# Optimization experiments

Measured on AMD Instinct MI355X. Metric: run time of the kernel, lower is better.

The kernel has to match this reference:

```python
import jax, jax.numpy as jnp
import numpy as np

E = 200_000       # num edges
A = 1_000_000     # num angle triplets
H = 128           # hidden_dim
BD = 8            # bilinear_dim
NR = 6            # num_radial_basis
NS = 7            # num_spherical_basis
MIN = 128         # message_in_dim
N_BEFORE = 1
N_AFTER = 2


def setup_inputs() -> dict:
    key = jax.random.key(0)
    ks = jax.random.split(key, 24)
    s = 0.05
    inp = {
        "distance_representation": jax.random.normal(ks[0], (E, NR), jnp.float32),
        "angle_representation": jax.random.normal(ks[1], (A, NS, NR), jnp.float32),
        "message": jax.random.normal(ks[2], (E, MIN), jnp.float32),
        "angle_index": jax.random.randint(ks[3], (2, A), 0, E),
        # parameters (stored as [in, out]; torch Linear applies x @ W.T)
        "W_dist": jax.random.normal(ks[4], (NR, H), jnp.float32) * s,
        "W_angle": jax.random.normal(ks[5], (NS * NR, BD), jnp.float32) * s,
        "W_src": jax.random.normal(ks[6], (MIN, H), jnp.float32) * s,
        "b_src": jnp.zeros((H,), jnp.float32),
        "W_tgt": jax.random.normal(ks[7], (MIN, H), jnp.float32) * s,
        "b_tgt": jnp.zeros((H,), jnp.float32),
        "W_bil": jax.random.normal(ks[8], (H, BD, H), jnp.float32) * (2.0 / H),
        "res_before_W": jax.random.normal(ks[9], (N_BEFORE, 2, H, H), jnp.float32) * s,
        "res_before_b": jnp.zeros((N_BEFORE, 2, H), jnp.float32),
        "W_skip": jax.random.normal(ks[10], (H, MIN), jnp.float32) * s,
        "b_skip": jnp.zeros((MIN,), jnp.float32),
        "res_after_W": jax.random.normal(ks[11], (N_AFTER, 2, MIN, MIN), jnp.float32) * s,
        "res_after_b": jnp.zeros((N_AFTER, 2, MIN), jnp.float32),
    }
    return inp


def _residual(x, Ws, bs, act):
    # x + act(L2(act(L1(x))))
    h = act(x @ Ws[0] + bs[0])
    h = act(h @ Ws[1] + bs[1])
    return x + h


def reference(distance_representation, angle_representation, message, angle_index,
              W_dist, W_angle, W_src, b_src, W_tgt, b_tgt, W_bil,
              res_before_W, res_before_b, W_skip, b_skip,
              res_after_W, res_after_b):
    act = jax.nn.silu
    num_edges = message.shape[0]
    num_angles = angle_index.shape[-1]

    d = distance_representation @ W_dist                       # [E, H]
    a = angle_representation.reshape(num_angles, -1) @ W_angle  # [A, BD]

    src_e, tgt_e = angle_index[0], angle_index[1]
    sm = message[src_e] @ W_src + b_src                        # [A, H] gather + linear
    sm = sm * d[tgt_e]                                         # [A, H]
    sm = jnp.einsum('ab,ah,ibh->ai', a, sm, W_bil)             # [A, H] bilinear

    agg = jax.ops.segment_sum(sm, tgt_e, num_segments=num_edges)  # [E, H] scatter-add

    x0 = message
    x = agg + (message @ W_tgt + b_tgt)
    for i in range(res_before_W.shape[0]):
        x = _residual(x, res_before_W[i], res_before_b[i], act)
    x = act(x @ W_skip + b_skip) + x0
    for i in range(res_after_W.shape[0]):
        x = _residual(x, res_after_W[i], res_after_b[i], act)
    return x
```

## Files before the change

### kernel.cpp

```cpp
#include <hip/hip_runtime.h>
#include <stdint.h>

#define E_N 200000
#define A_N 1000000

typedef short s16x8 __attribute__((ext_vector_type(8)));
typedef short s16x4 __attribute__((ext_vector_type(4)));
typedef float f32x4 __attribute__((ext_vector_type(4)));
typedef uint32_t u32x4 __attribute__((ext_vector_type(4)));
typedef uint32_t u32x2 __attribute__((ext_vector_type(2)));

__device__ __forceinline__ ushort f2bf(float f) {
  uint32_t x = __float_as_uint(f);
  uint32_t r = x + 0x7FFFu + ((x >> 16) & 1u);
  return (ushort)(r >> 16);
}

__device__ __forceinline__ float bf2f(ushort u) {
  return __uint_as_float(((uint32_t)u) << 16);
}

__device__ __forceinline__ uint32_t cvtpk(float lo, float hi) {
  uint32_t r;
  asm("v_cvt_pk_bf16_f32 %0, %1, %2" : "=v"(r) : "v"(lo), "v"(hi));
  return r;
}

__device__ __forceinline__ float silu_f(float v) {
  return v * (1.0f / (1.0f + __expf(-v)));
}

__device__ __forceinline__ int swz(int row, int h) {
  return row * 128 + (h ^ ((row & 7) << 3));
}

__device__ __forceinline__ int sws(int r, int c) {
  return r * 64 + ((c & 63) ^ ((r & 7) << 3));
}

__device__ __forceinline__ void exchCtoB(ushort* scw, int r15, int hi,
                                         const f32x4* xv, s16x8* st) {
  u32x2 pk[8];
#pragma unroll
  for (int nt = 0; nt < 8; nt++) {
    pk[nt][0] = cvtpk(xv[nt][0], xv[nt][1]);
    pk[nt][1] = cvtpk(xv[nt][2], xv[nt][3]);
  }
#pragma unroll
  for (int nt = 0; nt < 4; nt++)
    *(u32x2*)&scw[sws(r15, nt * 16 + hi * 4)] = pk[nt];
#pragma unroll
  for (int k = 0; k < 2; k++)
    st[k] = *(const s16x8*)&scw[sws(r15, k * 32 + hi * 8)];
#pragma unroll
  for (int nt = 4; nt < 8; nt++)
    *(u32x2*)&scw[sws(r15, nt * 16 + hi * 4)] = pk[nt];
#pragma unroll
  for (int k = 2; k < 4; k++)
    st[k] = *(const s16x8*)&scw[sws(r15, k * 32 + hi * 8)];
}

__device__ __forceinline__ void exchBtoC(ushort* scw, int r15, int hi,
                                         const s16x8* stv, u32x2* mc) {
#pragma unroll
  for (int k = 0; k < 2; k++)
    *(s16x8*)&scw[sws(r15, k * 32 + hi * 8)] = stv[k];
#pragma unroll
  for (int nt = 0; nt < 4; nt++)
    mc[nt] = *(const u32x2*)&scw[sws(r15, nt * 16 + hi * 4)];
#pragma unroll
  for (int k = 2; k < 4; k++)
    *(s16x8*)&scw[sws(r15, k * 32 + hi * 8)] = stv[k];
#pragma unroll
  for (int nt = 4; nt < 8; nt++)
    mc[nt] = *(const u32x2*)&scw[sws(r15, nt * 16 + hi * 4)];
}

__global__ __launch_bounds__(256) void k_prep(
    const float* __restrict__ Wbil, const float* __restrict__ Wsrc,
    const float* __restrict__ Wtgt, const float* __restrict__ WresB,
    const float* __restrict__ Wskip, const float* __restrict__ WresA,
    const float* __restrict__ bsrc, const float* __restrict__ btgt,
    const float* __restrict__ bresB, const float* __restrict__ bskip,
    const float* __restrict__ bresA,
    ushort* __restrict__ wg_bil, ushort* __restrict__ wg_lin,
    float* __restrict__ bias_tab) {
  int tid = blockIdx.x * 256 + threadIdx.x;
  if (tid < 8 * 16384) {
    int b = tid >> 14, r = tid & 16383;
    int i = r >> 7, h = r & 127;
    wg_bil[b * 16384 + swz(i, h)] = f2bf(Wbil[(i * 8 + b) * 128 + h]);
    return;
  }
  tid -= 8 * 16384;
  if (tid < 9 * 16384) {
    int s = tid >> 14, r = tid & 16383;
    int c = r >> 7, h = r & 127;
    const float* src;
    switch (s) {
      case 0: src = Wsrc; break;
      case 1: src = Wtgt; break;
      case 2: src = WresB; break;
      case 3: src = WresB + 16384; break;
      case 4: src = Wskip; break;
      case 5: src = WresA; break;
      case 6: src = WresA + 16384; break;
      case 7: src = WresA + 32768; break;
      default: src = WresA + 49152; break;
    }
    wg_lin[s * 16384 + swz(c, h)] = f2bf(src[h * 128 + c]);
    return;
  }
  tid -= 9 * 16384;
  if (tid < 9 * 128) {
    int s = tid >> 7, c = tid & 127;
    const float* src;
    switch (s) {
      case 0: src = bsrc; break;
      case 1: src = btgt; break;
      case 2: src = bresB; break;
      case 3: src = bresB + 128; break;
      case 4: src = bskip; break;
      case 5: src = bresA; break;
      case 6: src = bresA + 128; break;
      case 7: src = bresA + 256; break;
      default: src = bresA + 384; break;
    }
    bias_tab[s * 128 + c] = src[c];
  }
}

__global__ __launch_bounds__(256) void k_hist(const int* __restrict__ aidx,
                                              int* __restrict__ cnt) {
  int i = blockIdx.x * 256 + threadIdx.x;
  if (i < A_N) atomicAdd(&cnt[aidx[A_N + i]], 1);
}

__global__ __launch_bounds__(256) void k_scan1(const int* __restrict__ cnt,
                                               int* __restrict__ excl,
                                               int* __restrict__ bsum) {
  __shared__ int s[256];
  int t = threadIdx.x;
  int base = blockIdx.x * 1024 + t * 4;
  int v[4];
#pragma unroll
  for (int j = 0; j < 4; j++) v[j] = (base + j < E_N) ? cnt[base + j] : 0;
  int sum = v[0] + v[1] + v[2] + v[3];
  s[t] = sum;
  __syncthreads();
#pragma unroll
  for (int d = 1; d < 256; d <<= 1) {
    int x = (t >= d) ? s[t - d] : 0;
    __syncthreads();
    s[t] += x;
    __syncthreads();
  }
  int run = s[t] - sum;
#pragma unroll
  for (int j = 0; j < 4; j++) {
    if (base + j < E_N) excl[base + j] = run;
    run += v[j];
  }
  if (t == 255) bsum[blockIdx.x] = s[255];
}

__global__ __launch_bounds__(256) void k_scan2(int* __restrict__ bsum, int nb) {
  __shared__ int s[256];
  int t = threadIdx.x;
  int orig = (t < nb) ? bsum[t] : 0;
  s[t] = orig;
  __syncthreads();
#pragma unroll
  for (int d = 1; d < 256; d <<= 1) {
    int x = (t >= d) ? s[t - d] : 0;
    __syncthreads();
    s[t] += x;
    __syncthreads();
  }
  if (t < nb) bsum[t] = s[t] - orig;
}

__global__ __launch_bounds__(256) void k_scan3(const int* __restrict__ excl,
                                               const int* __restrict__ bsum,
                                               int* __restrict__ cursor) {
  int t = threadIdx.x;
  int base = blockIdx.x * 1024 + t * 4;
  int add = bsum[blockIdx.x];
#pragma unroll
  for (int j = 0; j < 4; j++)
    if (base + j < E_N) cursor[base + j] = excl[base + j] + add;
}

__global__ __launch_bounds__(256) void k_scatter(const int* __restrict__ aidx,
                                                 int* __restrict__ cursor,
                                                 int* __restrict__ perm,
                                                 int* __restrict__ ste) {
  int i = blockIdx.x * 256 + threadIdx.x;
  if (i < A_N) {
    int te = aidx[A_N + i];
    int pos = atomicAdd(&cursor[te], 1);
    perm[pos] = i;
    ste[pos] = te;
  }
}

__global__ __launch_bounds__(256) void k_angle(const float* __restrict__ ang,
                                               const float* __restrict__ Wang,
                                               float* __restrict__ a_ws) {
  __shared__ float rows[128 * 42];
  __shared__ float wbuf[42 * 8];
  int t = threadIdx.x;
  int tile0 = blockIdx.x * 128;
  int nrows = A_N - tile0; if (nrows > 128) nrows = 128;
  if (nrows == 128) {
    const f32x4* src = (const f32x4*)(ang + (size_t)tile0 * 42);
    f32x4* dst = (f32x4*)rows;
    for (int k = t; k < 1344; k += 256) dst[k] = src[k];
  } else {
    int cnt = nrows * 42;
    for (int k = t; k < cnt; k += 256) rows[k] = ang[(size_t)tile0 * 42 + k];
  }
  for (int k = t; k < 336; k += 256) wbuf[k] = Wang[k];
  __syncthreads();
  int row = t >> 1, half = t & 1;
  if (row < nrows) {
    float a0 = 0.f, a1 = 0.f, a2 = 0.f, a3 = 0.f;
    const float* rp = &rows[row * 42];
    const float* wp = &wbuf[half * 4];
#pragma unroll
    for (int k = 0; k < 42; k++) {
      float v = rp[k];
      a0 += v * wp[k * 8 + 0]; a1 += v * wp[k * 8 + 1];
      a2 += v * wp[k * 8 + 2]; a3 += v * wp[k * 8 + 3];
    }
    f32x4 o; o.x = a0; o.y = a1; o.z = a2; o.w = a3;
    *(f32x4*)&a_ws[(tile0 + row) * 8 + half * 4] = o;
  }
}

__global__ __launch_bounds__(256) void k_dist(const float* __restrict__ dist,
                                              const float* __restrict__ Wd,
                                              ushort* __restrict__ dtab) {
  __shared__ float w[6 * 128];
  int t = threadIdx.x;
  for (int k = t; k < 768; k += 256) w[k] = Wd[k];
  __syncthreads();
  int gid = blockIdx.x * 256 + t;
  int e = gid >> 2, q = gid & 3;
  if (e >= E_N) return;
  float dv[6];
#pragma unroll
  for (int r = 0; r < 6; r++) dv[r] = dist[e * 6 + r];
#pragma unroll
  for (int j = 0; j < 32; j += 4) {
    int c = q * 32 + j;
    s16x4 o;
#pragma unroll
    for (int jj = 0; jj < 4; jj++) {
      float s = 0.f;
#pragma unroll
      for (int r = 0; r < 6; r++) s += dv[r] * w[r * 128 + c + jj];
      o[jj] = (short)f2bf(s);
    }
    *(s16x4*)&dtab[e * 128 + c] = o;
  }
}

__global__ __launch_bounds__(512) void k_srcm(const float* __restrict__ msg,
                                              const ushort* __restrict__ wg_lin,
                                              const float* __restrict__ bias_tab,
                                              ushort* __restrict__ srcm) {
  __shared__ ushort xb[128 * 128];
  __shared__ ushort wb[16384];
  __shared__ float bias[128];
  int t = threadIdx.x;
  int tile0 = blockIdx.x * 128;
  const f32x4 Z4 = {0.f, 0.f, 0.f, 0.f};
  for (int off = t * 8; off < 16384; off += 4096)
    *(s16x8*)&wb[off] = *(const s16x8*)&wg_lin[off];
  if (t < 128) bias[t] = bias_tab[t];
  {
    int row = t >> 2, l = t & 3;
    int grow = tile0 + row;
#pragma unroll
    for (int j = 0; j < 8; j++) {
      int h = l * 32 + j * 4;
      s16x4 o; o[0] = 0; o[1] = 0; o[2] = 0; o[3] = 0;
      if (grow < E_N) {
        f32x4 v = *(const f32x4*)&msg[(size_t)grow * 128 + h];
        o[0] = (short)f2bf(v.x); o[1] = (short)f2bf(v.y);
        o[2] = (short)f2bf(v.z); o[3] = (short)f2bf(v.w);
      }
      *(s16x4*)&xb[swz(row, h)] = o;
    }
  }
  __syncthreads();
  int w = t >> 6, lane = t & 63;
  int rbase = w * 16;
  int arow = rbase + (lane & 15);
  int k0 = (lane >> 4) * 8;
  int r0 = (lane >> 4) * 4;
  f32x4 acc[8];
#pragma unroll
  for (int k = 0; k < 4; k++) {
    s16x8 af = *(const s16x8*)&xb[swz(arow, k * 32 + k0)];
#pragma unroll
    for (int nt = 0; nt < 8; nt++) {
      s16x8 bf = *(const s16x8*)&wb[swz(nt * 16 + (lane & 15), k * 32 + k0)];
      acc[nt] = __builtin_amdgcn_mfma_f32_16x16x32_bf16(af, bf, k == 0 ? Z4 : acc[nt], 0, 0, 0);
    }
  }
#pragma unroll
  for (int nt = 0; nt < 8; nt++) {
    int col = nt * 16 + (lane & 15);
    float bv = bias[col];
#pragma unroll
    for (int r = 0; r < 4; r++) {
      int grow = tile0 + rbase + r0 + r;
      if (grow < E_N) srcm[(size_t)grow * 128 + col] = f2bf(acc[nt][r] + bv);
    }
  }
}

__global__ __launch_bounds__(256) void k_bil(const int* __restrict__ aidx,
                                             const ushort* __restrict__ srcm,
                                             const ushort* __restrict__ dtab,
                                             const float* __restrict__ a_ws,
                                             const ushort* __restrict__ wg_bil,
                                             const int* __restrict__ perm,
                                             const int* __restrict__ ste,
                                             float* __restrict__ agg) {
  __shared__ ushort wb[2][16384];
  int t = threadIdx.x;
  int lane = t & 63, w = t >> 6;
  int tile0 = blockIdx.x * 128;
  int mb = w * 32;
  int r15 = lane & 15, hi = lane >> 4;
  int k0 = hi * 8;
  int r0 = hi * 4;
  const f32x4 Z4 = {0.f, 0.f, 0.f, 0.f};

  {
    const ushort* gs = wg_bil + w * 4096 + lane * 8;
    ushort* ls = &wb[0][w * 4096];
#pragma unroll
    for (int i = 0; i < 8; i++)
      __builtin_amdgcn_global_load_lds(
          (const __attribute__((address_space(1))) void*)(gs + i * 512),
          (__attribute__((address_space(3))) void*)(ls + i * 512), 16, 0, 0);
  }

  float smv[2][4][8];
  float av[2][8];
  int teo[2][4];
#pragma unroll
  for (int mt = 0; mt < 2; mt++) {
    int grow = tile0 + mb + mt * 16 + r15;
    int ok = (grow < A_N);
    int ga = ok ? perm[grow] : 0;
    int se = ok ? aidx[ga] : 0;
    int te = ok ? ste[grow] : 0;
    if (ok) {
      f32x4 a0 = *(const f32x4*)&a_ws[(size_t)ga * 8];
      f32x4 a1 = *(const f32x4*)&a_ws[(size_t)ga * 8 + 4];
#pragma unroll
      for (int j = 0; j < 4; j++) { av[mt][j] = a0[j]; av[mt][4 + j] = a1[j]; }
    } else {
#pragma unroll
      for (int j = 0; j < 8; j++) av[mt][j] = 0.f;
    }
#pragma unroll
    for (int k = 0; k < 4; k++) {
      s16x8 sv = *(const s16x8*)&srcm[(size_t)se * 128 + k * 32 + k0];
      s16x8 dv = *(const s16x8*)&dtab[(size_t)te * 128 + k * 32 + k0];
#pragma unroll
      for (int j = 0; j < 8; j++)
        smv[mt][k][j] = bf2f((ushort)sv[j]) * bf2f((ushort)dv[j]);
    }
#pragma unroll
    for (int r = 0; r < 4; r++) {
      int orow = tile0 + mb + mt * 16 + r0 + r;
      teo[mt][r] = (orow < A_N) ? ste[orow] : 0;
    }
  }

  f32x4 OUT[2][8];
#pragma unroll
  for (int mt = 0; mt < 2; mt++)
#pragma unroll
    for (int nt = 0; nt < 8; nt++) OUT[mt][nt] = Z4;

  __syncthreads();

#pragma unroll
  for (int b = 0; b < 8; b++) {
    int buf = b & 1;
    if (b < 7) {
      const ushort* gs = wg_bil + (b + 1) * 16384 + w * 4096 + lane * 8;
      ushort* ls = &wb[buf ^ 1][w * 4096];
#pragma unroll
      for (int i = 0; i < 8; i++)
        __builtin_amdgcn_global_load_lds(
            (const __attribute__((address_space(1))) void*)(gs + i * 512),
            (__attribute__((address_space(3))) void*)(ls + i * 512), 16, 0, 0);
    }
    float a0b = av[0][b], a1b = av[1][b];
#pragma unroll
    for (int k = 0; k < 4; k++) {
      u32x4 w0, w1;
#pragma unroll
      for (int jj = 0; jj < 4; jj++) {
        w0[jj] = cvtpk(a0b * smv[0][k][2 * jj], a0b * smv[0][k][2 * jj + 1]);
        w1[jj] = cvtpk(a1b * smv[1][k][2 * jj], a1b * smv[1][k][2 * jj + 1]);
      }
      s16x8 af0 = __builtin_bit_cast(s16x8, w0);
      s16x8 af1 = __builtin_bit_cast(s16x8, w1);
#pragma unroll
      for (int nt = 0; nt < 8; nt++) {
        s16x8 bf = *(const s16x8*)&wb[buf][swz(nt * 16 + r15, k * 32 + k0)];
        OUT[0][nt] = __builtin_amdgcn_mfma_f32_16x16x32_bf16(af0, bf, OUT[0][nt], 0, 0, 0);
        OUT[1][nt] = __builtin_amdgcn_mfma_f32_16x16x32_bf16(af1, bf, OUT[1][nt], 0, 0, 0);
      }
    }
    __syncthreads();
  }

#pragma unroll
  for (int mt = 0; mt < 2; mt++) {
    float acc[8];
    int cte = teo[mt][0];
#pragma unroll
    for (int nt = 0; nt < 8; nt++) acc[nt] = OUT[mt][nt][0];
#pragma unroll
    for (int r = 1; r < 4; r++) {
      int nte = teo[mt][r];
      if (nte == cte) {
#pragma unroll
        for (int nt = 0; nt < 8; nt++) acc[nt] += OUT[mt][nt][r];
      } else {
        float* base = &agg[(size_t)cte * 128];
#pragma unroll
        for (int nt = 0; nt < 8; nt++)
          unsafeAtomicAdd(base + nt * 16 + r15, acc[nt]);
        cte = nte;
#pragma unroll
        for (int nt = 0; nt < 8; nt++) acc[nt] = OUT[mt][nt][r];
      }
    }
    float* base = &agg[(size_t)cte * 128];
#pragma unroll
    for (int nt = 0; nt < 8; nt++)
      unsafeAtomicAdd(base + nt * 16 + r15, acc[nt]);
  }
}

__global__ __launch_bounds__(512) void k_postA(const float* __restrict__ msg,
                                               const float* __restrict__ agg,
                                               const ushort* __restrict__ wg_lin,
                                               const float* __restrict__ bias_tab,
                                               ushort* __restrict__ xmid) {
  __shared__ ushort wb[4][16384];
  __shared__ ushort sc[8][1024];
  __shared__ float bias[4][128];
  int t = threadIdx.x;
  int lane = t & 63, w = t >> 6;
  int r15 = lane & 15, hi = lane >> 4;
  ushort* scw = &sc[w][0];
  const f32x4 Z4 = {0.f, 0.f, 0.f, 0.f};

#pragma unroll
  for (int s = 0; s < 4; s++) {
    const ushort* gs = wg_lin + (s + 1) * 16384 + t * 8;
    ushort* ls = &wb[s][t * 8];
#pragma unroll
    for (int i = 0; i < 4; i++)
      __builtin_amdgcn_global_load_lds(
          (const __attribute__((address_space(1))) void*)(gs + i * 4096),
          (__attribute__((address_space(3))) void*)(ls + i * 4096), 16, 0, 0);
  }
  if (t < 128) {
#pragma unroll
    for (int s = 0; s < 4; s++) bias[s][t] = bias_tab[(s + 1) * 128 + t];
  }
  __syncthreads();

#pragma unroll 1
  for (int tb = blockIdx.x; tb < 1563; tb += 521) {
    int r = tb * 128 + w * 16 + r15;
    bool ok = r < E_N;
    size_t gb = (size_t)r * 128;

    s16x8 st[4], mg[4];
#pragma unroll
    for (int k = 0; k < 4; k++) {
      f32x4 v0 = Z4, v1 = Z4;
      if (ok) {
        v0 = *(const f32x4*)&msg[gb + k * 32 + hi * 8];
        v1 = *(const f32x4*)&msg[gb + k * 32 + hi * 8 + 4];
      }
      u32x4 p;
      p[0] = cvtpk(v0.x, v0.y); p[1] = cvtpk(v0.z, v0.w);
      p[2] = cvtpk(v1.x, v1.y); p[3] = cvtpk(v1.z, v1.w);
      st[k] = __builtin_bit_cast(s16x8, p);
      mg[k] = st[k];
    }
    f32x4 ag[8];
#pragma unroll
    for (int nt = 0; nt < 8; nt++)
      ag[nt] = ok ? *(const f32x4*)&agg[gb + nt * 16 + hi * 4] : Z4;

    f32x4 xr[8], xv[8], C[8];

#pragma unroll
    for (int k = 0; k < 4; k++)
#pragma unroll
      for (int nt = 0; nt < 8; nt++) {
        s16x8 af = *(const s16x8*)&wb[0][swz(nt * 16 + r15, k * 32 + hi * 8)];
        C[nt] = __builtin_amdgcn_mfma_f32_16x16x32_bf16(af, st[k], k == 0 ? ag[nt] : C[nt], 0, 0, 0);
      }
#pragma unroll
    for (int nt = 0; nt < 8; nt++) {
      f32x4 bv = *(const f32x4*)&bias[0][nt * 16 + hi * 4];
#pragma unroll
      for (int q = 0; q < 4; q++) xv[nt][q] = C[nt][q] + bv[q];
      xr[nt] = xv[nt];
    }
    exchCtoB(scw, r15, hi, xv, st);

#pragma unroll
    for (int k = 0; k < 4; k++)
#pragma unroll
      for (int nt = 0; nt < 8; nt++) {
        s16x8 af = *(const s16x8*)&wb[1][swz(nt * 16 + r15, k * 32 + hi * 8)];
        C[nt] = __builtin_amdgcn_mfma_f32_16x16x32_bf16(af, st[k], k == 0 ? Z4 : C[nt], 0, 0, 0);
      }
#pragma unroll
    for (int nt = 0; nt < 8; nt++) {
      f32x4 bv = *(const f32x4*)&bias[1][nt * 16 + hi * 4];
#pragma unroll
      for (int q = 0; q < 4; q++) xv[nt][q] = silu_f(C[nt][q] + bv[q]);
    }
    exchCtoB(scw, r15, hi, xv, st);

#pragma unroll
    for (int k = 0; k < 4; k++)
#pragma unroll
      for (int nt = 0; nt < 8; nt++) {
        s16x8 af = *(const s16x8*)&wb[2][swz(nt * 16 + r15, k * 32 + hi * 8)];
        C[nt] = __builtin_amdgcn_mfma_f32_16x16x32_bf16(af, st[k], k == 0 ? Z4 : C[nt], 0, 0, 0);
      }
#pragma unroll
    for (int nt = 0; nt < 8; nt++) {
      f32x4 bv = *(const f32x4*)&bias[2][nt * 16 + hi * 4];
#pragma unroll
      for (int q = 0; q < 4; q++) xv[nt][q] = xr[nt][q] + silu_f(C[nt][q] + bv[q]);
    }
    exchCtoB(scw, r15, hi, xv, st);

#pragma unroll
    for (int k = 0; k < 4; k++)
#pragma unroll
      for (int nt = 0; nt < 8; nt++) {
        s16x8 af = *(const s16x8*)&wb[3][swz(nt * 16 + r15, k * 32 + hi * 8)];
        C[nt] = __builtin_amdgcn_mfma_f32_16x16x32_bf16(af, st[k], k == 0 ? Z4 : C[nt], 0, 0, 0);
      }
    u32x2 mc[8];
    exchBtoC(scw, r15, hi, mg, mc);
#pragma unroll
    for (int nt = 0; nt < 8; nt++) {
      f32x4 bv = *(const f32x4*)&bias[3][nt * 16 + hi * 4];
      f32x4 m0;
      m0[0] = __uint_as_float(mc[nt][0] << 16);
      m0[1] = __uint_as_float(mc[nt][0] & 0xffff0000u);
      m0[2] = __uint_as_float(mc[nt][1] << 16);
      m0[3] = __uint_as_float(mc[nt][1] & 0xffff0000u);
      u32x2 pk;
      float o0 = silu_f(C[nt][0] + bv[0]) + m0[0];
      float o1 = silu_f(C[nt][1] + bv[1]) + m0[1];
      float o2 = silu_f(C[nt][2] + bv[2]) + m0[2];
      float o3 = silu_f(C[nt][3] + bv[3]) + m0[3];
      pk[0] = cvtpk(o0, o1);
      pk[1] = cvtpk(o2, o3);
      if (ok) *(u32x2*)&xmid[gb + nt * 16 + hi * 4] = pk;
    }
  }
}

__global__ __launch_bounds__(512) void k_postB(const ushort* __restrict__ xmid,
                                               const ushort* __restrict__ wg_lin,
                                               const float* __restrict__ bias_tab,
                                               float* __restrict__ xout) {
  __shared__ ushort wb[4][16384];
  __shared__ ushort sc[8][1024];
  __shared__ float bias[4][128];
  int t = threadIdx.x;
  int lane = t & 63, w = t >> 6;
  int r15 = lane & 15, hi = lane >> 4;
  ushort* scw = &sc[w][0];
  const f32x4 Z4 = {0.f, 0.f, 0.f, 0.f};

#pragma unroll
  for (int s = 0; s < 4; s++) {
    const ushort* gs = wg_lin + (s + 5) * 16384 + t * 8;
    ushort* ls = &wb[s][t * 8];
#pragma unroll
    for (int i = 0; i < 4; i++)
      __builtin_amdgcn_global_load_lds(
          (const __attribute__((address_space(1))) void*)(gs + i * 4096),
          (__attribute__((address_space(3))) void*)(ls + i * 4096), 16, 0, 0);
  }
  if (t < 128) {
#pragma unroll
    for (int s = 0; s < 4; s++) bias[s][t] = bias_tab[(s + 5) * 128 + t];
  }
  __syncthreads();

#pragma unroll 1
  for (int tb = blockIdx.x; tb < 1563; tb += 521) {
    int r = tb * 128 + w * 16 + r15;
    bool ok = r < E_N;
    size_t gb = (size_t)r * 128;

    s16x8 st[4];
#pragma unroll
    for (int k = 0; k < 4; k++) {
      s16x8 z; u32x4 zz; zz[0] = 0; zz[1] = 0; zz[2] = 0; zz[3] = 0;
      z = __builtin_bit_cast(s16x8, zz);
      st[k] = ok ? *(const s16x8*)&xmid[gb + k * 32 + hi * 8] : z;
    }
    u32x2 mc[8];
    exchBtoC(scw, r15, hi, st, mc);
    f32x4 xr[8], xv[8], C[8];
#pragma unroll
    for (int nt = 0; nt < 8; nt++) {
      xr[nt][0] = __uint_as_float(mc[nt][0] << 16);
      xr[nt][1] = __uint_as_float(mc[nt][0] & 0xffff0000u);
      xr[nt][2] = __uint_as_float(mc[nt][1] << 16);
      xr[nt][3] = __uint_as_float(mc[nt][1] & 0xffff0000u);
    }

#pragma unroll
    for (int k = 0; k < 4; k++)
#pragma unroll
      for (int nt = 0; nt < 8; nt++) {
        s16x8 af = *(const s16x8*)&wb[0][swz(nt * 16 + r15, k * 32 + hi * 8)];
        C[nt] = __builtin_amdgcn_mfma_f32_16x16x32_bf16(af, st[k], k == 0 ? Z4 : C[nt], 0, 0, 0);
      }
#pragma unroll
    for (int nt = 0; nt < 8; nt++) {
      f32x4 bv = *(const f32x4*)&bias[0][nt * 16 + hi * 4];
#pragma unroll
      for (int q = 0; q < 4; q++) xv[nt][q] = silu_f(C[nt][q] + bv[q]);
    }
    exchCtoB(scw, r15, hi, xv, st);

#pragma unroll
    for (int k = 0; k < 4; k++)
#pragma unroll
      for (int nt = 0; nt < 8; nt++) {
        s16x8 af = *(const s16x8*)&wb[1][swz(nt * 16 + r15, k * 32 + hi * 8)];
        C[nt] = __builtin_amdgcn_mfma_f32_16x16x32_bf16(af, st[k], k == 0 ? Z4 : C[nt], 0, 0, 0);
      }
#pragma unroll
    for (int nt = 0; nt < 8; nt++) {
      f32x4 bv = *(const f32x4*)&bias[1][nt * 16 + hi * 4];
#pragma unroll
      for (int q = 0; q < 4; q++) xv[nt][q] = xr[nt][q] + silu_f(C[nt][q] + bv[q]);
      xr[nt] = xv[nt];
    }
    exchCtoB(scw, r15, hi, xv, st);

#pragma unroll
    for (int k = 0; k < 4; k++)
#pragma unroll
      for (int nt = 0; nt < 8; nt++) {
        s16x8 af = *(const s16x8*)&wb[2][swz(nt * 16 + r15, k * 32 + hi * 8)];
        C[nt] = __builtin_amdgcn_mfma_f32_16x16x32_bf16(af, st[k], k == 0 ? Z4 : C[nt], 0, 0, 0);
      }
#pragma unroll
    for (int nt = 0; nt < 8; nt++) {
      f32x4 bv = *(const f32x4*)&bias[2][nt * 16 + hi * 4];
#pragma unroll
      for (int q = 0; q < 4; q++) xv[nt][q] = silu_f(C[nt][q] + bv[q]);
    }
    exchCtoB(scw, r15, hi, xv, st);

#pragma unroll
    for (int k = 0; k < 4; k++)
#pragma unroll
      for (int nt = 0; nt < 8; nt++) {
        s16x8 af = *(const s16x8*)&wb[3][swz(nt * 16 + r15, k * 32 + hi * 8)];
        C[nt] = __builtin_amdgcn_mfma_f32_16x16x32_bf16(af, st[k], k == 0 ? Z4 : C[nt], 0, 0, 0);
      }
#pragma unroll
    for (int nt = 0; nt < 8; nt++) {
      f32x4 bv = *(const f32x4*)&bias[3][nt * 16 + hi * 4];
      f32x4 o;
#pragma unroll
      for (int q = 0; q < 4; q++) o[q] = xr[nt][q] + silu_f(C[nt][q] + bv[q]);
      if (ok) *(f32x4*)&xout[gb + nt * 16 + hi * 4] = o;
    }
  }
}

extern "C" void kernel_launch(void* const* d_in, const int* in_sizes, int n_in,
                              void* d_out, int out_size, void* d_ws, size_t ws_size,
                              hipStream_t stream) {
  const float* dist  = (const float*)d_in[0];
  const float* ang   = (const float*)d_in[1];
  const float* msg   = (const float*)d_in[2];
  const int*   aidx  = (const int*)d_in[3];
  const float* Wd    = (const float*)d_in[4];
  const float* Wang  = (const float*)d_in[5];
  const float* Wsrc  = (const float*)d_in[6];
  const float* bsrc  = (const float*)d_in[7];
  const float* Wtgt  = (const float*)d_in[8];
  const float* btgt  = (const float*)d_in[9];
  const float* Wbil  = (const float*)d_in[10];
  const float* WresB = (const float*)d_in[11];
  const float* bresB = (const float*)d_in[12];
  const float* Wskip = (const float*)d_in[13];
  const float* bskip = (const float*)d_in[14];
  const float* WresA = (const float*)d_in[15];
  const float* bresA = (const float*)d_in[16];

  char* ws = (char*)d_ws;
  ushort* srcm_bf  = (ushort*)(ws + 0);
  ushort* dtab_bf  = (ushort*)(ws + 51200000LL);
  float*  a_ws     = (float*)(ws + 102400000LL);
  ushort* wg_bil   = (ushort*)(ws + 134400000LL);
  ushort* wg_lin   = (ushort*)(ws + 134662144LL);
  float*  bias_tab = (float*)(ws + 134957056LL);
  int*    cnt      = (int*)(ws + 134961664LL);
  int*    cursor   = (int*)(ws + 135761664LL);
  int*    excl     = (int*)(ws + 136561664LL);
  int*    bsum     = (int*)(ws + 137361664LL);
  int*    perm     = (int*)(ws + 137362688LL);
  int*    ste      = (int*)(ws + 141362688LL);
  ushort* xmid     = (ushort*)(ws + 145362688LL);
  float*  agg      = (float*)d_out;

  (void)in_sizes; (void)n_in; (void)out_size; (void)ws_size;

  const int NSCAN = (E_N + 1023) / 1024;

  hipMemsetAsync(d_out, 0, (size_t)E_N * 128 * 4, stream);
  hipMemsetAsync(cnt, 0, (size_t)E_N * 4, stream);
  k_prep<<<1093, 256, 0, stream>>>(Wbil, Wsrc, Wtgt, WresB, Wskip, WresA,
                                   bsrc, btgt, bresB, bskip, bresA,
                                   wg_bil, wg_lin, bias_tab);
  k_hist<<<3907, 256, 0, stream>>>(aidx, cnt);
  k_scan1<<<NSCAN, 256, 0, stream>>>(cnt, excl, bsum);
  k_scan2<<<1, 256, 0, stream>>>(bsum, NSCAN);
  k_scan3<<<NSCAN, 256, 0, stream>>>(excl, bsum, cursor);
  k_scatter<<<3907, 256, 0, stream>>>(aidx, cursor, perm, ste);
  k_angle<<<7813, 256, 0, stream>>>(ang, Wang, a_ws);
  k_dist<<<3125, 256, 0, stream>>>(dist, Wd, dtab_bf);
  k_srcm<<<1563, 512, 0, stream>>>(msg, wg_lin, bias_tab, srcm_bf);
  k_bil<<<7813, 256, 0, stream>>>(aidx, srcm_bf, dtab_bf, a_ws, wg_bil,
                                  perm, ste, agg);
  k_postA<<<521, 512, 0, stream>>>(msg, agg, wg_lin, bias_tab, xmid);
  k_postB<<<521, 512, 0, stream>>>(xmid, wg_lin, bias_tab, (float*)d_out);
}
```

Baseline: 850.2 us.

## Single-buffer bilinear weights and re-grid post-MLP kernels with 12-wave blocks

k_bil drops the LDS double buffer to a single 32KB slice and declares 4 blocks per CU in its launch bounds, adding a sync before each weight reload, so more blocks can be resident at the cost of weaker overlap between weight loads and MFMA work. k_postA/k_postB move to 768-thread blocks (12 waves) with a per-wave 16-row tile loop, so each block loads its 128KB of weights once and amortises it over more work. They also drop the bounds checks, since E divides evenly into 16-row tiles. The LDS exchange used to rebuild the residual input is replaced by re-reading message/xmid straight from global memory. That trades LDS traffic for extra global reads and takes the fp32 message in the skip add instead of its bf16 rounding.

```diff
diff --git a/kernel.cpp b/kernel.cpp
--- a/kernel.cpp
+++ b/kernel.cpp
@@ -58,22 +58,6 @@
 #pragma unroll
   for (int k = 2; k < 4; k++)
     st[k] = *(const s16x8*)&scw[sws(r15, k * 32 + hi * 8)];
-}
-
-__device__ __forceinline__ void exchBtoC(ushort* scw, int r15, int hi,
-                                         const s16x8* stv, u32x2* mc) {
-#pragma unroll
-  for (int k = 0; k < 2; k++)
-    *(s16x8*)&scw[sws(r15, k * 32 + hi * 8)] = stv[k];
-#pragma unroll
-  for (int nt = 0; nt < 4; nt++)
-    mc[nt] = *(const u32x2*)&scw[sws(r15, nt * 16 + hi * 4)];
-#pragma unroll
-  for (int k = 2; k < 4; k++)
-    *(s16x8*)&scw[sws(r15, k * 32 + hi * 8)] = stv[k];
-#pragma unroll
-  for (int nt = 4; nt < 8; nt++)
-    mc[nt] = *(const u32x2*)&scw[sws(r15, nt * 16 + hi * 4)];
 }
 
 __global__ __launch_bounds__(256) void k_prep(
@@ -322,15 +306,15 @@
   }
 }
 
-__global__ __launch_bounds__(256) void k_bil(const int* __restrict__ aidx,
-                                             const ushort* __restrict__ srcm,
-                                             const ushort* __restrict__ dtab,
-                                             const float* __restrict__ a_ws,
-                                             const ushort* __restrict__ wg_bil,
-                                             const int* __restrict__ perm,
-                                             const int* __restrict__ ste,
-                                             float* __restrict__ agg) {
-  __shared__ ushort wb[2][16384];
+__global__ __launch_bounds__(256, 4) void k_bil(const int* __restrict__ aidx,
+                                                const ushort* __restrict__ srcm,
+                                                const ushort* __restrict__ dtab,
+                                                const float* __restrict__ a_ws,
+                                                const ushort* __restrict__ wg_bil,
+                                                const int* __restrict__ perm,
+                                                const int* __restrict__ ste,
+                                                float* __restrict__ agg) {
+  __shared__ ushort wb[16384];
   int t = threadIdx.x;
   int lane = t & 63, w = t >> 6;
   int tile0 = blockIdx.x * 128;
@@ -342,7 +326,7 @@
 
   {
     const ushort* gs = wg_bil + w * 4096 + lane * 8;
-    ushort* ls = &wb[0][w * 4096];
+    ushort* ls = &wb[w * 4096];
 #pragma unroll
     for (int i = 0; i < 8; i++)
       __builtin_amdgcn_global_load_lds(
@@ -394,35 +378,35 @@
 
 #pragma unroll
   for (int b = 0; b < 8; b++) {
-    int buf = b & 1;
+    float a0b = av[0][b], a1b = av[1][b];
+#pragma unroll
+    for (int k = 0; k < 4; k++) {
+      u32x4 w0, w1;
+#pragma unroll
+      for (int jj = 0; jj < 4; jj++) {
+        w0[jj] = cvtpk(a0b * smv[0][k][2 * jj], a0b * smv[0][k][2 * jj + 1]);
+        w1[jj] = cvtpk(a1b * smv[1][k][2 * jj], a1b * smv[1][k][2 * jj + 1]);
+      }
+      s16x8 af0 = __builtin_bit_cast(s16x8, w0);
+      s16x8 af1 = __builtin_bit_cast(s16x8, w1);
+#pragma unroll
+      for (int nt = 0; nt < 8; nt++) {
+        s16x8 bf = *(const s16x8*)&wb[swz(nt * 16 + r15, k * 32 + k0)];
+        OUT[0][nt] = __builtin_amdgcn_mfma_f32_16x16x32_bf16(af0, bf, OUT[0][nt], 0, 0, 0);
+        OUT[1][nt] = __builtin_amdgcn_mfma_f32_16x16x32_bf16(af1, bf, OUT[1][nt], 0, 0, 0);
+      }
+    }
     if (b < 7) {
+      __syncthreads();
       const ushort* gs = wg_bil + (b + 1) * 16384 + w * 4096 + lane * 8;
-      ushort* ls = &wb[buf ^ 1][w * 4096];
+      ushort* ls = &wb[w * 4096];
 #pragma unroll
       for (int i = 0; i < 8; i++)
         __builtin_amdgcn_global_load_lds(
             (const __attribute__((address_space(1))) void*)(gs + i * 512),
             (__attribute__((address_space(3))) void*)(ls + i * 512), 16, 0, 0);
-    }
-    float a0b = av[0][b], a1b = av[1][b];
-#pragma unroll
-    for (int k = 0; k < 4; k++) {
-      u32x4 w0, w1;
-#pragma unroll
-      for (int jj = 0; jj < 4; jj++) {
-        w0[jj] = cvtpk(a0b * smv[0][k][2 * jj], a0b * smv[0][k][2 * jj + 1]);
-        w1[jj] = cvtpk(a1b * smv[1][k][2 * jj], a1b * smv[1][k][2 * jj + 1]);
-      }
-      s16x8 af0 = __builtin_bit_cast(s16x8, w0);
-      s16x8 af1 = __builtin_bit_cast(s16x8, w1);
-#pragma unroll
-      for (int nt = 0; nt < 8; nt++) {
-        s16x8 bf = *(const s16x8*)&wb[buf][swz(nt * 16 + r15, k * 32 + k0)];
-        OUT[0][nt] = __builtin_amdgcn_mfma_f32_16x16x32_bf16(af0, bf, OUT[0][nt], 0, 0, 0);
-        OUT[1][nt] = __builtin_amdgcn_mfma_f32_16x16x32_bf16(af1, bf, OUT[1][nt], 0, 0, 0);
-      }
-    }
-    __syncthreads();
+      __syncthreads();
+    }
   }
 
 #pragma unroll
@@ -454,13 +438,13 @@
   }
 }
 
-__global__ __launch_bounds__(512) void k_postA(const float* __restrict__ msg,
-                                               const float* __restrict__ agg,
-                                               const ushort* __restrict__ wg_lin,
-                                               const float* __restrict__ bias_tab,
-                                               ushort* __restrict__ xmid) {
+__global__ __launch_bounds__(768, 3) void k_postA(const float* __restrict__ msg,
+                                                  const float* __restrict__ agg,
+                                                  const ushort* __restrict__ wg_lin,
+                                                  const float* __restrict__ bias_tab,
+                                                  ushort* __restrict__ xmid) {
   __shared__ ushort wb[4][16384];
-  __shared__ ushort sc[8][1024];
+  __shared__ ushort sc[12][1024];
   __shared__ float bias[4][128];
   int t = threadIdx.x;
   int lane = t & 63, w = t >> 6;
@@ -468,15 +452,12 @@
   ushort* scw = &sc[w][0];
   const f32x4 Z4 = {0.f, 0.f, 0.f, 0.f};
 
-#pragma unroll
-  for (int s = 0; s < 4; s++) {
-    const ushort* gs = wg_lin + (s + 1) * 16384 + t * 8;
-    ushort* ls = &wb[s][t * 8];
-#pragma unroll
-    for (int i = 0; i < 4; i++)
-      __builtin_amdgcn_global_load_lds(
-          (const __attribute__((address_space(1))) void*)(gs + i * 4096),
-          (__attribute__((address_space(3))) void*)(ls + i * 4096), 16, 0, 0);
+  for (int c = w; c < 128; c += 12) {
+    const ushort* gs = wg_lin + 16384 + c * 512 + lane * 8;
+    ushort* ls = &wb[0][0] + c * 512 + lane * 8;
+    __builtin_amdgcn_global_load_lds(
+        (const __attribute__((address_space(1))) void*)gs,
+        (__attribute__((address_space(3))) void*)ls, 16, 0, 0);
   }
   if (t < 128) {
 #pragma unroll
@@ -485,29 +466,23 @@
   __syncthreads();
 
 #pragma unroll 1
-  for (int tb = blockIdx.x; tb < 1563; tb += 521) {
-    int r = tb * 128 + w * 16 + r15;
-    bool ok = r < E_N;
-    size_t gb = (size_t)r * 128;
-
-    s16x8 st[4], mg[4];
+  for (int tt = blockIdx.x * 12 + w; tt < 12500; tt += 3120) {
+    size_t gb = ((size_t)tt * 16 + r15) * 128;
+
+    s16x8 st[4];
 #pragma unroll
     for (int k = 0; k < 4; k++) {
-      f32x4 v0 = Z4, v1 = Z4;
-      if (ok) {
-        v0 = *(const f32x4*)&msg[gb + k * 32 + hi * 8];
-        v1 = *(const f32x4*)&msg[gb + k * 32 + hi * 8 + 4];
-      }
+      f32x4 v0 = *(const f32x4*)&msg[gb + k * 32 + hi * 8];
+      f32x4 v1 = *(const f32x4*)&msg[gb + k * 32 + hi * 8 + 4];
       u32x4 p;
       p[0] = cvtpk(v0.x, v0.y); p[1] = cvtpk(v0.z, v0.w);
       p[2] = cvtpk(v1.x, v1.y); p[3] = cvtpk(v1.z, v1.w);
       st[k] = __builtin_bit_cast(s16x8, p);
-      mg[k] = st[k];
     }
     f32x4 ag[8];
 #pragma unroll
     for (int nt = 0; nt < 8; nt++)
-      ag[nt] = ok ? *(const f32x4*)&agg[gb + nt * 16 + hi * 4] : Z4;
+      ag[nt] = *(const f32x4*)&agg[gb + nt * 16 + hi * 4];
 
     f32x4 xr[8], xv[8], C[8];
 
@@ -564,16 +539,10 @@
         s16x8 af = *(const s16x8*)&wb[3][swz(nt * 16 + r15, k * 32 + hi * 8)];
         C[nt] = __builtin_amdgcn_mfma_f32_16x16x32_bf16(af, st[k], k == 0 ? Z4 : C[nt], 0, 0, 0);
       }
-    u32x2 mc[8];
-    exchBtoC(scw, r15, hi, mg, mc);
 #pragma unroll
     for (int nt = 0; nt < 8; nt++) {
       f32x4 bv = *(const f32x4*)&bias[3][nt * 16 + hi * 4];
-      f32x4 m0;
-      m0[0] = __uint_as_float(mc[nt][0] << 16);
-      m0[1] = __uint_as_float(mc[nt][0] & 0xffff0000u);
-      m0[2] = __uint_as_float(mc[nt][1] << 16);
-      m0[3] = __uint_as_float(mc[nt][1] & 0xffff0000u);
+      f32x4 m0 = *(const f32x4*)&msg[gb + nt * 16 + hi * 4];
       u32x2 pk;
       float o0 = silu_f(C[nt][0] + bv[0]) + m0[0];
       float o1 = silu_f(C[nt][1] + bv[1]) + m0[1];
@@ -581,17 +550,17 @@
       float o3 = silu_f(C[nt][3] + bv[3]) + m0[3];
       pk[0] = cvtpk(o0, o1);
       pk[1] = cvtpk(o2, o3);
-      if (ok) *(u32x2*)&xmid[gb + nt * 16 + hi * 4] = pk;
-    }
-  }
-}
-
-__global__ __launch_bounds__(512) void k_postB(const ushort* __restrict__ xmid,
-                                               const ushort* __restrict__ wg_lin,
-                                               const float* __restrict__ bias_tab,
-                                               float* __restrict__ xout) {
+      *(u32x2*)&xmid[gb + nt * 16 + hi * 4] = pk;
+    }
+  }
+}
+
+__global__ __launch_bounds__(768, 3) void k_postB(const ushort* __restrict__ xmid,
+                                                  const ushort* __restrict__ wg_lin,
+                                                  const float* __restrict__ bias_tab,
+                                                  float* __restrict__ xout) {
   __shared__ ushort wb[4][16384];
-  __shared__ ushort sc[8][1024];
+  __shared__ ushort sc[12][1024];
   __shared__ float bias[4][128];
   int t = threadIdx.x;
   int lane = t & 63, w = t >> 6;
@@ -599,15 +568,12 @@
   ushort* scw = &sc[w][0];
   const f32x4 Z4 = {0.f, 0.f, 0.f, 0.f};
 
-#pragma unroll
-  for (int s = 0; s < 4; s++) {
-    const ushort* gs = wg_lin + (s + 5) * 16384 + t * 8;
-    ushort* ls = &wb[s][t * 8];
-#pragma unroll
-    for (int i = 0; i < 4; i++)
-      __builtin_amdgcn_global_load_lds(
-          (const __attribute__((address_space(1))) void*)(gs + i * 4096),
-          (__attribute__((address_space(3))) void*)(ls + i * 4096), 16, 0, 0);
+  for (int c = w; c < 128; c += 12) {
+    const ushort* gs = wg_lin + 5 * 16384 + c * 512 + lane * 8;
+    ushort* ls = &wb[0][0] + c * 512 + lane * 8;
+    __builtin_amdgcn_global_load_lds(
+        (const __attribute__((address_space(1))) void*)gs,
+        (__attribute__((address_space(3))) void*)ls, 16, 0, 0);
   }
   if (t < 128) {
 #pragma unroll
@@ -616,27 +582,21 @@
   __syncthreads();
 
 #pragma unroll 1
-  for (int tb = blockIdx.x; tb < 1563; tb += 521) {
-    int r = tb * 128 + w * 16 + r15;
-    bool ok = r < E_N;
-    size_t gb = (size_t)r * 128;
+  for (int tt = blockIdx.x * 12 + w; tt < 12500; tt += 3120) {
+    size_t gb = ((size_t)tt * 16 + r15) * 128;
 
     s16x8 st[4];
 #pragma unroll
-    for (int k = 0; k < 4; k++) {
-      s16x8 z; u32x4 zz; zz[0] = 0; zz[1] = 0; zz[2] = 0; zz[3] = 0;
-      z = __builtin_bit_cast(s16x8, zz);
-      st[k] = ok ? *(const s16x8*)&xmid[gb + k * 32 + hi * 8] : z;
-    }
-    u32x2 mc[8];
-    exchBtoC(scw, r15, hi, st, mc);
+    for (int k = 0; k < 4; k++)
+      st[k] = *(const s16x8*)&xmid[gb + k * 32 + hi * 8];
     f32x4 xr[8], xv[8], C[8];
 #pragma unroll
     for (int nt = 0; nt < 8; nt++) {
-      xr[nt][0] = __uint_as_float(mc[nt][0] << 16);
-      xr[nt][1] = __uint_as_float(mc[nt][0] & 0xffff0000u);
-      xr[nt][2] = __uint_as_float(mc[nt][1] << 16);
-      xr[nt][3] = __uint_as_float(mc[nt][1] & 0xffff0000u);
+      u32x2 mc = *(const u32x2*)&xmid[gb + nt * 16 + hi * 4];
+      xr[nt][0] = __uint_as_float(mc[0] << 16);
+      xr[nt][1] = __uint_as_float(mc[0] & 0xffff0000u);
+      xr[nt][2] = __uint_as_float(mc[1] << 16);
+      xr[nt][3] = __uint_as_float(mc[1] & 0xffff0000u);
     }
 
 #pragma unroll
@@ -698,7 +658,7 @@
       f32x4 o;
 #pragma unroll
       for (int q = 0; q < 4; q++) o[q] = xr[nt][q] + silu_f(C[nt][q] + bv[q]);
-      if (ok) *(f32x4*)&xout[gb + nt * 16 + hi * 4] = o;
+      *(f32x4*)&xout[gb + nt * 16 + hi * 4] = o;
     }
   }
 }
@@ -759,6 +719,6 @@
   k_srcm<<<1563, 512, 0, stream>>>(msg, wg_lin, bias_tab, srcm_bf);
   k_bil<<<7813, 256, 0, stream>>>(aidx, srcm_bf, dtab_bf, a_ws, wg_bil,
                                   perm, ste, agg);
-  k_postA<<<521, 512, 0, stream>>>(msg, agg, wg_lin, bias_tab, xmid);
-  k_postB<<<521, 512, 0, stream>>>(xmid, wg_lin, bias_tab, (float*)d_out);
-}
+  k_postA<<<260, 768, 0, stream>>>(msg, agg, wg_lin, bias_tab, xmid);
+  k_postB<<<260, 768, 0, stream>>>(xmid, wg_lin, bias_tab, (float*)d_out);
+}
```

After: 1.371 ms. 1.61x slower.

## Switch bilinear path to fp16 with packed multiplies and single LDS buffer

Applied to the files above, without the earlier changes.

Converts the srcm, dtab and bilinear weight tables from bf16 to fp16. The bilinear kernel now does the elementwise products with packed v_pk_mul_f16 instead of fp32 multiplies plus bf16 repacking, and feeds fp16 MFMA. It also drops the double-buffered LDS weight tile for a single buffer and sets a 3-blocks-per-CU launch bound, aiming for fewer VALU ops and registers and higher occupancy. In exchange, the next weight slice is loaded between barriers with no overlap against compute, and fp16 has a narrower range that could overflow.

```diff
diff --git a/kernel.cpp b/kernel.cpp
--- a/kernel.cpp
+++ b/kernel.cpp
@@ -1,4 +1,5 @@
 #include <hip/hip_runtime.h>
+#include <hip/hip_fp16.h>
 #include <stdint.h>
 
 #define E_N 200000
@@ -9,6 +10,7 @@
 typedef float f32x4 __attribute__((ext_vector_type(4)));
 typedef uint32_t u32x4 __attribute__((ext_vector_type(4)));
 typedef uint32_t u32x2 __attribute__((ext_vector_type(2)));
+typedef _Float16 f16x8 __attribute__((ext_vector_type(8)));
 
 __device__ __forceinline__ ushort f2bf(float f) {
   uint32_t x = __float_as_uint(f);
@@ -16,13 +18,19 @@
   return (ushort)(r >> 16);
 }
 
-__device__ __forceinline__ float bf2f(ushort u) {
-  return __uint_as_float(((uint32_t)u) << 16);
+__device__ __forceinline__ ushort f2h(float f) {
+  return __half_as_ushort(__float2half(f));
 }
 
 __device__ __forceinline__ uint32_t cvtpk(float lo, float hi) {
   uint32_t r;
   asm("v_cvt_pk_bf16_f32 %0, %1, %2" : "=v"(r) : "v"(lo), "v"(hi));
+  return r;
+}
+
+__device__ __forceinline__ uint32_t pkmul(uint32_t a, uint32_t b) {
+  uint32_t r;
+  asm("v_pk_mul_f16 %0, %1, %2" : "=v"(r) : "v"(a), "v"(b));
   return r;
 }
 
@@ -89,7 +97,7 @@
   if (tid < 8 * 16384) {
     int b = tid >> 14, r = tid & 16383;
     int i = r >> 7, h = r & 127;
-    wg_bil[b * 16384 + swz(i, h)] = f2bf(Wbil[(i * 8 + b) * 128 + h]);
+    wg_bil[b * 16384 + swz(i, h)] = f2h(Wbil[(i * 8 + b) * 128 + h]);
     return;
   }
   tid -= 8 * 16384;
@@ -260,7 +268,7 @@
       float s = 0.f;
 #pragma unroll
       for (int r = 0; r < 6; r++) s += dv[r] * w[r * 128 + c + jj];
-      o[jj] = (short)f2bf(s);
+      o[jj] = (short)f2h(s);
     }
     *(s16x4*)&dtab[e * 128 + c] = o;
   }
@@ -317,20 +325,20 @@
 #pragma unroll
     for (int r = 0; r < 4; r++) {
       int grow = tile0 + rbase + r0 + r;
-      if (grow < E_N) srcm[(size_t)grow * 128 + col] = f2bf(acc[nt][r] + bv);
-    }
-  }
-}
-
-__global__ __launch_bounds__(256) void k_bil(const int* __restrict__ aidx,
-                                             const ushort* __restrict__ srcm,
-                                             const ushort* __restrict__ dtab,
-                                             const float* __restrict__ a_ws,
-                                             const ushort* __restrict__ wg_bil,
-                                             const int* __restrict__ perm,
-                                             const int* __restrict__ ste,
-                                             float* __restrict__ agg) {
-  __shared__ ushort wb[2][16384];
+      if (grow < E_N) srcm[(size_t)grow * 128 + col] = f2h(acc[nt][r] + bv);
+    }
+  }
+}
+
+__global__ __launch_bounds__(256, 3) void k_bil(const int* __restrict__ aidx,
+                                                const ushort* __restrict__ srcm,
+                                                const ushort* __restrict__ dtab,
+                                                const float* __restrict__ a_ws,
+                                                const ushort* __restrict__ wg_bil,
+                                                const int* __restrict__ perm,
+                                                const int* __restrict__ ste,
+                                                float* __restrict__ agg) {
+  __shared__ ushort wb[16384];
   int t = threadIdx.x;
   int lane = t & 63, w = t >> 6;
   int tile0 = blockIdx.x * 128;
@@ -342,7 +350,7 @@
 
   {
     const ushort* gs = wg_bil + w * 4096 + lane * 8;
-    ushort* ls = &wb[0][w * 4096];
+    ushort* ls = &wb[w * 4096];
 #pragma unroll
     for (int i = 0; i < 8; i++)
       __builtin_amdgcn_global_load_lds(
@@ -350,8 +358,8 @@
           (__attribute__((address_space(3))) void*)(ls + i * 512), 16, 0, 0);
   }
 
-  float smv[2][4][8];
-  float av[2][8];
+  u32x4 smv[2][4];
+  uint32_t avd[2][8];
   int teo[2][4];
 #pragma unroll
   for (int mt = 0; mt < 2; mt++) {
@@ -364,18 +372,21 @@
       f32x4 a0 = *(const f32x4*)&a_ws[(size_t)ga * 8];
       f32x4 a1 = *(const f32x4*)&a_ws[(size_t)ga * 8 + 4];
 #pragma unroll
-      for (int j = 0; j < 4; j++) { av[mt][j] = a0[j]; av[mt][4 + j] = a1[j]; }
+      for (int j = 0; j < 4; j++) {
+        uint32_t h0 = f2h(a0[j]), h1 = f2h(a1[j]);
+        avd[mt][j] = (h0 << 16) | h0;
+        avd[mt][4 + j] = (h1 << 16) | h1;
+      }
     } else {
 #pragma unroll
-      for (int j = 0; j < 8; j++) av[mt][j] = 0.f;
+      for (int j = 0; j < 8; j++) avd[mt][j] = 0u;
     }
 #pragma unroll
     for (int k = 0; k < 4; k++) {
-      s16x8 sv = *(const s16x8*)&srcm[(size_t)se * 128 + k * 32 + k0];
-      s16x8 dv = *(const s16x8*)&dtab[(size_t)te * 128 + k * 32 + k0];
-#pragma unroll
-      for (int j = 0; j < 8; j++)
-        smv[mt][k][j] = bf2f((ushort)sv[j]) * bf2f((ushort)dv[j]);
+      u32x4 sv = *(const u32x4*)&srcm[(size_t)se * 128 + k * 32 + k0];
+      u32x4 dv = *(const u32x4*)&dtab[(size_t)te * 128 + k * 32 + k0];
+#pragma unroll
+      for (int j = 0; j < 4; j++) smv[mt][k][j] = pkmul(sv[j], dv[j]);
     }
 #pragma unroll
     for (int r = 0; r < 4; r++) {
@@ -394,35 +405,35 @@
 
 #pragma unroll
   for (int b = 0; b < 8; b++) {
-    int buf = b & 1;
+    uint32_t a0b = avd[0][b], a1b = avd[1][b];
+#pragma unroll
+    for (int k = 0; k < 4; k++) {
+      u32x4 p0, p1;
+#pragma unroll
+      for (int j = 0; j < 4; j++) {
+        p0[j] = pkmul(smv[0][k][j], a0b);
+        p1[j] = pkmul(smv[1][k][j], a1b);
+      }
+      f16x8 af0 = __builtin_bit_cast(f16x8, p0);
+      f16x8 af1 = __builtin_bit_cast(f16x8, p1);
+#pragma unroll
+      for (int nt = 0; nt < 8; nt++) {
+        f16x8 bf = *(const f16x8*)&wb[swz(nt * 16 + r15, k * 32 + k0)];
+        OUT[0][nt] = __builtin_amdgcn_mfma_f32_16x16x32_f16(af0, bf, OUT[0][nt], 0, 0, 0);
+        OUT[1][nt] = __builtin_amdgcn_mfma_f32_16x16x32_f16(af1, bf, OUT[1][nt], 0, 0, 0);
+      }
+    }
     if (b < 7) {
+      __syncthreads();
       const ushort* gs = wg_bil + (b + 1) * 16384 + w * 4096 + lane * 8;
-      ushort* ls = &wb[buf ^ 1][w * 4096];
+      ushort* ls = &wb[w * 4096];
 #pragma unroll
       for (int i = 0; i < 8; i++)
         __builtin_amdgcn_global_load_lds(
             (const __attribute__((address_space(1))) void*)(gs + i * 512),
             (__attribute__((address_space(3))) void*)(ls + i * 512), 16, 0, 0);
-    }
-    float a0b = av[0][b], a1b = av[1][b];
-#pragma unroll
-    for (int k = 0; k < 4; k++) {
-      u32x4 w0, w1;
-#pragma unroll
-      for (int jj = 0; jj < 4; jj++) {
-        w0[jj] = cvtpk(a0b * smv[0][k][2 * jj], a0b * smv[0][k][2 * jj + 1]);
-        w1[jj] = cvtpk(a1b * smv[1][k][2 * jj], a1b * smv[1][k][2 * jj + 1]);
-      }
-      s16x8 af0 = __builtin_bit_cast(s16x8, w0);
-      s16x8 af1 = __builtin_bit_cast(s16x8, w1);
-#pragma unroll
-      for (int nt = 0; nt < 8; nt++) {
-        s16x8 bf = *(const s16x8*)&wb[buf][swz(nt * 16 + r15, k * 32 + k0)];
-        OUT[0][nt] = __builtin_amdgcn_mfma_f32_16x16x32_bf16(af0, bf, OUT[0][nt], 0, 0, 0);
-        OUT[1][nt] = __builtin_amdgcn_mfma_f32_16x16x32_bf16(af1, bf, OUT[1][nt], 0, 0, 0);
-      }
-    }
-    __syncthreads();
+      __syncthreads();
+    }
   }
 
 #pragma unroll
@@ -725,8 +736,8 @@
   const float* bresA = (const float*)d_in[16];
 
   char* ws = (char*)d_ws;
-  ushort* srcm_bf  = (ushort*)(ws + 0);
-  ushort* dtab_bf  = (ushort*)(ws + 51200000LL);
+  ushort* srcm_f16 = (ushort*)(ws + 0);
+  ushort* dtab_f16 = (ushort*)(ws + 51200000LL);
   float*  a_ws     = (float*)(ws + 102400000LL);
   ushort* wg_bil   = (ushort*)(ws + 134400000LL);
   ushort* wg_lin   = (ushort*)(ws + 134662144LL);
@@ -755,9 +766,9 @@
   k_scan3<<<NSCAN, 256, 0, stream>>>(excl, bsum, cursor);
   k_scatter<<<3907, 256, 0, stream>>>(aidx, cursor, perm, ste);
   k_angle<<<7813, 256, 0, stream>>>(ang, Wang, a_ws);
-  k_dist<<<3125, 256, 0, stream>>>(dist, Wd, dtab_bf);
-  k_srcm<<<1563, 512, 0, stream>>>(msg, wg_lin, bias_tab, srcm_bf);
-  k_bil<<<7813, 256, 0, stream>>>(aidx, srcm_bf, dtab_bf, a_ws, wg_bil,
+  k_dist<<<3125, 256, 0, stream>>>(dist, Wd, dtab_f16);
+  k_srcm<<<1563, 512, 0, stream>>>(msg, wg_lin, bias_tab, srcm_f16);
+  k_bil<<<7813, 256, 0, stream>>>(aidx, srcm_f16, dtab_f16, a_ws, wg_bil,
                                   perm, ste, agg);
   k_postA<<<521, 512, 0, stream>>>(msg, agg, wg_lin, bias_tab, xmid);
   k_postB<<<521, 512, 0, stream>>>(xmid, wg_lin, bias_tab, (float*)d_out);
```

Result: no change. 840.1 us (-1.2%).
